# Optimization experiments

Hardware: AMD Instinct MI355X
Metric: run time of the kernel (lower is better)

## Reference

```python
import jax, jax.numpy as jnp
import numpy as np

GROUPS = 4  # init kwarg


def setup_inputs() -> dict:
    key = jax.random.key(0)
    k1, k2, k3, k4 = jax.random.split(key, 4)
    B, S, D, H = 4, 4096, 256, 10
    # 0.02 scale on weights keeps unscaled QK^T logits in a sane range
    # (original torch code uses raw randn weights and applies NO 1/sqrt(d)
    # scaling inside group_attention, which saturates softmax).
    return {
        "x": jax.random.normal(k1, (B, S, D), dtype=jnp.float32),
        "Wq": jax.random.normal(k2, (H, D, D), dtype=jnp.float32) * 0.02,
        "Wk": jax.random.normal(k3, (H, D, D), dtype=jnp.float32) * 0.02,
        "Wo": jax.random.normal(k4, (D, H * D), dtype=jnp.float32) * 0.02,
    }


def reference(x, Wq, Wk, Wo):
    # x: [B,S,D]; Wq/Wk: [H,D,D]; Wo: [D, H*D] (nn.Linear weight layout)
    H, D, _ = Wq.shape
    B, S, _ = x.shape
    G = GROUPS
    C = S // G  # chunk length

    Q = jnp.einsum('bsd,hde->hbse', x, Wq)  # [H,B,S,D]
    K = jnp.einsum('bsd,hde->hbse', x, Wk)
    # Faithful to source bug: V is projected with wk weights -> V == K

    Qg = Q.reshape(H, B, G, C, D)
    KVg = jnp.roll(K.reshape(H, B, G, C, D), shift=-1, axis=2)  # chunk i attends chunk (i+1)%G

    # NOTE: original applies NO scaling to logits (scale arg unused)
    S_ = jnp.einsum('hbgqd,hbgkd->hbgqk', Qg, KVg)   # [H,B,G,C,C]
    P = jax.nn.softmax(S_, axis=-1)
    O = jnp.einsum('hbgqk,hbgkd->hbgqd', P, KVg)     # [H,B,G,C,D]

    # concat heads on feature dim: [B,S,H*D]
    out = O.reshape(H, B, S, D).transpose(1, 2, 0, 3).reshape(B, S, H * D)
    return jnp.einsum('bsk,dk->bsd', out, Wo)  # final Linear (no bias)
```

## Files before the change

### kernel.cpp

```cpp
#include <hip/hip_runtime.h>

typedef float f32x4 __attribute__((ext_vector_type(4)));
typedef float f32x16 __attribute__((ext_vector_type(16)));
typedef short s16x8 __attribute__((ext_vector_type(8)));
typedef unsigned int u32;

#define BSZ 4
#define SEQ 4096
#define DIM 256
#define NH 10
#define NG 4
#define CHK 1024
#define BS_TOT 16384
#define HD 2560
#define LOG2E 1.44269504f

__device__ __forceinline__ unsigned short f2bf(float f) {
    unsigned int u = __builtin_bit_cast(unsigned int, f);
    u = (u + 0x7fffu + ((u >> 16) & 1u)) >> 16;
    return (unsigned short)u;
}

__device__ __forceinline__ void gload_lds16(const unsigned short* g, unsigned short* l) {
    __builtin_amdgcn_global_load_lds((const __attribute__((address_space(1))) u32*)g,
                                     (__attribute__((address_space(3))) u32*)l, 16, 0, 0);
}

__device__ __forceinline__ u32 cvtpk_bf16(float lo, float hi) {
    u32 r;
    asm("v_cvt_pk_bf16_f32 %0, %1, %2" : "=v"(r) : "v"(lo), "v"(hi));
    return r;
}


__global__ __launch_bounds__(256) void cast_f32_bf16(const float* __restrict__ s,
                                                     unsigned short* __restrict__ d, int n) {
    long i = 4L * (blockIdx.x * 256 + threadIdx.x);
    if (i < n) {
        float4 v = *(const float4*)(s + i);
        ushort4 o;
        o.x = f2bf(v.x); o.y = f2bf(v.y); o.z = f2bf(v.z); o.w = f2bf(v.w);
        *(ushort4*)(d + i) = o;
    }
}

__global__ __launch_bounds__(256) void transpose_cast_w(const float* __restrict__ Wq,
                                                        const float* __restrict__ Wk,
                                                        unsigned short* __restrict__ wqt,
                                                        unsigned short* __restrict__ wkt) {
    const float* W = (blockIdx.z & 1) ? Wk : Wq;
    unsigned short* Wt = (blockIdx.z & 1) ? wkt : wqt;
    int h = blockIdx.z >> 1;
    __shared__ float tile[32][33];
    int d0 = blockIdx.x * 32, e0 = blockIdx.y * 32;
    int tx = threadIdx.x & 31, ty = threadIdx.x >> 5;
    const float* Wh = W + (long)h * 65536;
    unsigned short* Wth = Wt + (long)h * 65536;
#pragma unroll
    for (int r = ty; r < 32; r += 8) tile[r][tx] = Wh[(long)(d0 + r) * 256 + e0 + tx];
    __syncthreads();
#pragma unroll
    for (int r = ty; r < 32; r += 8) Wth[(long)(e0 + r) * 256 + d0 + tx] = f2bf(tile[tx][r]);
}


__device__ __forceinline__ void gemm_body(const unsigned short* __restrict__ A, long lda,
                                          const unsigned short* __restrict__ Bt, long ldb,
                                          unsigned short* Cb, float* Cf, long ldc,
                                          int K, bool accum, long mbase,
                                          unsigned short* KTo, float cscale) {
    __shared__ unsigned short As[64 * 40];
    __shared__ unsigned short Bs[256 * 40];
    const int t = threadIdx.x;
    const int w = t >> 6, l = t & 63, lr = l & 15, lg = l >> 4;

    f32x4 acc[16];
#pragma unroll
    for (int i = 0; i < 16; i++) acc[i] = (f32x4){0.f, 0.f, 0.f, 0.f};

    const int ar = t >> 2, akc = (t & 3) * 8;

    for (int k0 = 0; k0 < K; k0 += 32) {
        *(s16x8*)(&As[ar * 40 + akc]) = *(const s16x8*)(A + (mbase + ar) * lda + k0 + akc);
#pragma unroll
        for (int s = 0; s < 4; s++) {
            int n = s * 64 + (t >> 2);
            *(s16x8*)(&Bs[n * 40 + akc]) = *(const s16x8*)(Bt + (long)n * ldb + k0 + akc);
        }
        __syncthreads();
        s16x8 af = *(const s16x8*)(&As[(w * 16 + lr) * 40 + lg * 8]);
        __builtin_amdgcn_s_setprio(1);
#pragma unroll
        for (int nt = 0; nt < 16; nt++) {
            s16x8 bf = *(const s16x8*)(&Bs[(nt * 16 + lr) * 40 + lg * 8]);
            acc[nt] = __builtin_amdgcn_mfma_f32_16x16x32_bf16(af, bf, acc[nt], 0, 0, 0);
        }
        __builtin_amdgcn_s_setprio(0);
        __syncthreads();
    }
    long m0 = mbase + w * 16 + lg * 4;
#pragma unroll
    for (int nt = 0; nt < 16; nt++) {
        int col = nt * 16 + lr;
#pragma unroll
        for (int r = 0; r < 4; r++) {
            long idx = (m0 + r) * ldc + col;
            if (Cb) {
                Cb[idx] = f2bf(acc[nt][r] * cscale);
            } else {
                float v = acc[nt][r];
                if (accum) v += Cf[idx];
                Cf[idx] = v;
            }
        }
    }
    if (KTo) {
        int bg = (int)(m0 >> 10);
        int key0 = (int)(m0 & 1023);
        unsigned short* base = KTo + (long)bg * (256 * 1024)
                             + (long)(key0 >> 5) * (256 * 32) + (key0 & 31);
#pragma unroll
        for (int nt = 0; nt < 16; nt++) {
            int col = nt * 16 + lr;
            ushort4 v;
            v.x = f2bf(acc[nt][0]); v.y = f2bf(acc[nt][1]);
            v.z = f2bf(acc[nt][2]); v.w = f2bf(acc[nt][3]);
            *(ushort4*)(base + (long)col * 32) = v;
        }
    }
}

__global__ __launch_bounds__(256) void proj_kernel(const unsigned short* __restrict__ xb,
                                                   const unsigned short* __restrict__ wqt,
                                                   const unsigned short* __restrict__ wkt,
                                                   unsigned short* Qb, unsigned short* Kb,
                                                   unsigned short* KTb,
                                                   int h0, long headStrideOut, long headStrideKT) {
    int h = h0 + blockIdx.y;
    bool isK = (blockIdx.z != 0);
    const unsigned short* Bt = (isK ? wkt : wqt) + (long)h * 65536;
    unsigned short* C = (isK ? Kb : Qb) + (long)blockIdx.y * headStrideOut;
    unsigned short* KTo = isK ? (KTb + (long)blockIdx.y * headStrideKT) : nullptr;
    gemm_body(xb, 256, Bt, 256, C, nullptr, 256, 256, false, (long)blockIdx.x * 64, KTo,
              isK ? 1.0f : LOG2E);
}

__global__ __launch_bounds__(256) void final_kernel(const unsigned short* __restrict__ Ob, long lda,
                                                    const unsigned short* __restrict__ wob, long ldb,
                                                    float* out, int K, int accum) {
    gemm_body(Ob, lda, wob, ldb, nullptr, out, 256, K, accum != 0, (long)blockIdx.x * 64,
              nullptr, 1.0f);
}


__global__ __launch_bounds__(256, 3) void proj128(const unsigned short* __restrict__ xb,
                                                  const unsigned short* __restrict__ wqt,
                                                  const unsigned short* __restrict__ wkt,
                                                  unsigned short* __restrict__ Qb,
                                                  unsigned short* __restrict__ Kb,
                                                  unsigned short* __restrict__ KTb,
                                                  long headStrideOut, long headStrideKT) {
    __shared__ unsigned short As[2][128 * 32];
    __shared__ unsigned short Bs[2][128 * 32];

    const int lb = blockIdx.x;
    const int logical = (lb & 7) * 640 + (lb >> 3);
    const int x = logical / 40;
    const int u = logical - x * 40;
    const int mat = u >> 1, ntile = u & 1;
    const int h = mat >> 1;
    const bool isK = (mat & 1) != 0;
    const float cs = isK ? 1.0f : LOG2E;

    const unsigned short* A = xb;
    const unsigned short* Bt = (isK ? wkt : wqt) + (long)h * 65536 + (long)ntile * 128 * 256;
    unsigned short* C = (isK ? Kb : Qb) + (long)h * headStrideOut;
    unsigned short* KTo = isK ? (KTb + (long)h * headStrideKT) : nullptr;
    const long mbase = (long)x * 128;
    const int ncol0 = ntile * 128;

    const int t = threadIdx.x, w = t >> 6, l = t & 63, lr = l & 15, lg = l >> 4;
    const int wm = w >> 1, wn = w & 1;

    int sOff[2];
#pragma unroll
    for (int i = 0; i < 2; i++) {
        int row = w * 32 + i * 16 + (l >> 2);
        int cs2 = (l & 3) ^ (row & 3);
        sOff[i] = row * 256 + cs2 * 8;
    }

    f32x4 acc[4][4];
#pragma unroll
    for (int i = 0; i < 4; i++)
#pragma unroll
        for (int j = 0; j < 4; j++) acc[i][j] = (f32x4){0.f, 0.f, 0.f, 0.f};

#define PSTAGE(buf, k0) do {                                                     \
        _Pragma("unroll")                                                        \
        for (int i = 0; i < 2; i++)                                              \
            gload_lds16(A + mbase * 256 + (k0) + sOff[i],                        \
                        &As[buf][(w * 32 + i * 16) * 32]);                       \
        _Pragma("unroll")                                                        \
        for (int i = 0; i < 2; i++)                                              \
            gload_lds16(Bt + (k0) + sOff[i],                                     \
                        &Bs[buf][(w * 32 + i * 16) * 32]);                       \
    } while (0)

    PSTAGE(0, 0);
    __syncthreads();
    int cur = 0;
    for (int ks = 0; ks < 8; ++ks) {
        if (ks < 7) PSTAGE(cur ^ 1, (ks + 1) * 32);
        s16x8 a[4], b[4];
#pragma unroll
        for (int mf = 0; mf < 4; mf++) {
            int row = wm * 64 + mf * 16 + lr;
            a[mf] = *(const s16x8*)(&As[cur][row * 32 + (lg ^ (row & 3)) * 8]);
        }
#pragma unroll
        for (int nf = 0; nf < 4; nf++) {
            int row = wn * 64 + nf * 16 + lr;
            b[nf] = *(const s16x8*)(&Bs[cur][row * 32 + (lg ^ (row & 3)) * 8]);
        }
        __builtin_amdgcn_s_setprio(1);
#pragma unroll
        for (int mf = 0; mf < 4; mf++)
#pragma unroll
            for (int nf = 0; nf < 4; nf++)
                acc[mf][nf] = __builtin_amdgcn_mfma_f32_16x16x32_bf16(a[mf], b[nf], acc[mf][nf], 0, 0, 0);
        __builtin_amdgcn_s_setprio(0);
        __syncthreads();
        cur ^= 1;
    }
#undef PSTAGE

    long m0 = mbase + wm * 64 + lg * 4;
#pragma unroll
    for (int mf = 0; mf < 4; mf++) {
        long mrow = m0 + mf * 16;
#pragma unroll
        for (int nf = 0; nf < 4; nf++) {
            int col = ncol0 + wn * 64 + nf * 16 + lr;
#pragma unroll
            for (int r = 0; r < 4; r++) C[(mrow + r) * 256 + col] = f2bf(acc[mf][nf][r] * cs);
        }
    }
    if (KTo) {
#pragma unroll
        for (int mf = 0; mf < 4; mf++) {
            long key = m0 + mf * 16;
            int bg = (int)(key >> 10), k0i = (int)(key & 1023);
            unsigned short* base = KTo + (long)bg * (256 * 1024)
                                 + (long)(k0i >> 5) * (256 * 32) + (k0i & 31);
#pragma unroll
            for (int nf = 0; nf < 4; nf++) {
                int col = ncol0 + wn * 64 + nf * 16 + lr;
                ushort4 v;
                v.x = f2bf(acc[mf][nf][0]); v.y = f2bf(acc[mf][nf][1]);
                v.z = f2bf(acc[mf][nf][2]); v.w = f2bf(acc[mf][nf][3]);
                *(ushort4*)(base + (long)col * 32) = v;
            }
        }
    }
}


__global__ __launch_bounds__(256, 3) void final128(const unsigned short* __restrict__ Ob,
                                                   long headStride,
                                                   const unsigned short* __restrict__ wob,
                                                   float* __restrict__ out) {
    __shared__ unsigned short As[2][128 * 32];
    __shared__ unsigned short Bs[2][128 * 32];

    const int lb = blockIdx.x;
    const int logical = (lb & 7) * 32 + (lb >> 3);
    const int x = logical >> 1, ntile = logical & 1;
    const long mbase = (long)x * 128;
    const int ncol0 = ntile * 128;
    const unsigned short* Bt = wob + (long)ncol0 * HD;

    const int t = threadIdx.x, w = t >> 6, l = t & 63, lr = l & 15, lg = l >> 4;
    const int wm = w >> 1, wn = w & 1;

    int sOffA[2], sOffB[2];
#pragma unroll
    for (int i = 0; i < 2; i++) {
        int row = w * 32 + i * 16 + (l >> 2);
        int cs2 = (l & 3) ^ (row & 3);
        sOffA[i] = row * 256 + cs2 * 8;
        sOffB[i] = row * HD + cs2 * 8;
    }

    f32x4 acc[4][4];
#pragma unroll
    for (int i = 0; i < 4; i++)
#pragma unroll
        for (int j = 0; j < 4; j++) acc[i][j] = (f32x4){0.f, 0.f, 0.f, 0.f};

#define FSTAGE(buf, k0) do {                                                     \
        const unsigned short* Asrc = Ob + (long)((k0) >> 8) * headStride         \
                                   + mbase * 256 + ((k0) & 255);                 \
        _Pragma("unroll")                                                        \
        for (int i = 0; i < 2; i++)                                              \
            gload_lds16(Asrc + sOffA[i], &As[buf][(w * 32 + i * 16) * 32]);      \
        _Pragma("unroll")                                                        \
        for (int i = 0; i < 2; i++)                                              \
            gload_lds16(Bt + (k0) + sOffB[i], &Bs[buf][(w * 32 + i * 16) * 32]); \
    } while (0)

    FSTAGE(0, 0);
    __syncthreads();
    int cur = 0;
    for (int ks = 0; ks < 80; ++ks) {
        if (ks < 79) FSTAGE(cur ^ 1, (ks + 1) * 32);
        s16x8 a[4], b[4];
#pragma unroll
        for (int mf = 0; mf < 4; mf++) {
            int row = wm * 64 + mf * 16 + lr;
            a[mf] = *(const s16x8*)(&As[cur][row * 32 + (lg ^ (row & 3)) * 8]);
        }
#pragma unroll
        for (int nf = 0; nf < 4; nf++) {
            int row = wn * 64 + nf * 16 + lr;
            b[nf] = *(const s16x8*)(&Bs[cur][row * 32 + (lg ^ (row & 3)) * 8]);
        }
        __builtin_amdgcn_s_setprio(1);
#pragma unroll
        for (int mf = 0; mf < 4; mf++)
#pragma unroll
            for (int nf = 0; nf < 4; nf++)
                acc[mf][nf] = __builtin_amdgcn_mfma_f32_16x16x32_bf16(a[mf], b[nf], acc[mf][nf], 0, 0, 0);
        __builtin_amdgcn_s_setprio(0);
        __syncthreads();
        cur ^= 1;
    }
#undef FSTAGE

    long m0 = mbase + wm * 64 + lg * 4;
#pragma unroll
    for (int mf = 0; mf < 4; mf++) {
        long mrow = m0 + mf * 16;
#pragma unroll
        for (int nf = 0; nf < 4; nf++) {
            int col = ncol0 + wn * 64 + nf * 16 + lr;
#pragma unroll
            for (int r = 0; r < 4; r++) out[(mrow + r) * 256 + col] = acc[mf][nf][r];
        }
    }
}


__global__ __launch_bounds__(256, 2) void attn_kernel(const unsigned short* __restrict__ Qb,
                                                      const unsigned short* __restrict__ Kb,
                                                      long headStrideQK,
                                                      const unsigned short* __restrict__ KTg,
                                                      long headStrideKT,
                                                      unsigned short* __restrict__ Ob,
                                                      long ldo, long colStride,
                                                      int chunkPerXcd) {
    const int lb = blockIdx.x;
    const int logical = (lb & 7) * chunkPerXcd + (lb >> 3);
    const int bx = logical & 7;
    const int by = (logical >> 3) & 15;
    const int h = logical >> 7;

    const unsigned short* Q = Qb + (long)h * headStrideQK;
    const unsigned short* Kp = Kb + (long)h * headStrideQK;
    const unsigned short* KT = KTg + (long)h * headStrideKT;
    unsigned short* O = Ob + (long)h * colStride;
    const int b = by >> 2, g = by & 3;
    const long qrow0 = (long)b * SEQ + (long)g * CHK + (long)bx * 128;
    const long krow0 = (long)b * SEQ + (long)((g + 1) & 3) * CHK;
    const unsigned short* KTc = KT + (long)(b * NG + ((g + 1) & 3)) * (256 * 1024);

    __shared__ unsigned short Krm[2][32 * 256];
    __shared__ unsigned short KTt[2][256 * 32];

    const int t = threadIdx.x;
    const int w = t >> 6, l = t & 63, l31 = l & 31, hi = l >> 5;

    s16x8 qf[16];
    {
        const unsigned short* qp = Q + (qrow0 + w * 32 + l31) * 256 + hi * 8;
#pragma unroll
        for (int s = 0; s < 16; s++) qf[s] = *(const s16x8*)(qp + s * 16);
    }

    f32x16 o[8];
#pragma unroll
    for (int i = 0; i < 8; i++)
#pragma unroll
        for (int j = 0; j < 16; j++) o[i][j] = 0.f;
    float l_part = 0.f;

    int kOff[4], tOff[4];
#pragma unroll
    for (int i = 0; i < 4; i++) {
        int rowK = w * 8 + i * 2 + (l >> 5);
        kOff[i] = rowK * 256 + (((l & 31) ^ (rowK & 7)) * 8);
        int rowT = w * 64 + i * 16 + (l >> 2);
        tOff[i] = rowT * 32 + (((l & 3) ^ ((rowT >> 1) & 3)) * 8);
    }

#define STAGE(buf, kt_) do {                                                    \
        const unsigned short* Ksrc = Kp + (krow0 + (long)(kt_) * 32) * 256;     \
        const unsigned short* Tsrc = KTc + (long)(kt_) * (32 * 256);            \
        _Pragma("unroll")                                                       \
        for (int i = 0; i < 4; i++)                                             \
            gload_lds16(Ksrc + kOff[i], &Krm[buf][(w * 8 + i * 2) * 256]);      \
        _Pragma("unroll")                                                       \
        for (int i = 0; i < 4; i++)                                             \
            gload_lds16(Tsrc + tOff[i], &KTt[buf][(w * 64 + i * 16) * 32]);     \
    } while (0)

    STAGE(0, 0);
    __syncthreads();
    int cur = 0;

    for (int kt = 0; kt < 32; ++kt) {
        if (kt < 31) STAGE(cur ^ 1, kt + 1);

        f32x16 st;
#pragma unroll
        for (int j = 0; j < 16; j++) st[j] = 0.f;
        __builtin_amdgcn_s_setprio(1);
#pragma unroll
        for (int ks = 0; ks < 16; ks++) {
            int col = ((2 * ks + hi) ^ (l31 & 7)) * 8;
            s16x8 kf = *(const s16x8*)(&Krm[cur][l31 * 256 + col]);
            st = __builtin_amdgcn_mfma_f32_32x32x16_bf16(kf, qf[ks], st, 0, 0, 0);
        }
        __builtin_amdgcn_s_setprio(0);

        u32 c0, c1, c2, c3, c4, c5, c6, c7;
        {
            float pa0 = __builtin_amdgcn_exp2f(st[0]),  pa1 = __builtin_amdgcn_exp2f(st[1]);
            float pa2 = __builtin_amdgcn_exp2f(st[2]),  pa3 = __builtin_amdgcn_exp2f(st[3]);
            float pa4 = __builtin_amdgcn_exp2f(st[4]),  pa5 = __builtin_amdgcn_exp2f(st[5]);
            float pa6 = __builtin_amdgcn_exp2f(st[6]),  pa7 = __builtin_amdgcn_exp2f(st[7]);
            float pa8 = __builtin_amdgcn_exp2f(st[8]),  pa9 = __builtin_amdgcn_exp2f(st[9]);
            float paA = __builtin_amdgcn_exp2f(st[10]), paB = __builtin_amdgcn_exp2f(st[11]);
            float paC = __builtin_amdgcn_exp2f(st[12]), paD = __builtin_amdgcn_exp2f(st[13]);
            float paE = __builtin_amdgcn_exp2f(st[14]), paF = __builtin_amdgcn_exp2f(st[15]);
            l_part += (((pa0 + pa1) + (pa2 + pa3)) + ((pa4 + pa5) + (pa6 + pa7)))
                    + (((pa8 + pa9) + (paA + paB)) + ((paC + paD) + (paE + paF)));
            c0 = cvtpk_bf16(pa0, pa1); c1 = cvtpk_bf16(pa2, pa3);
            c2 = cvtpk_bf16(pa4, pa5); c3 = cvtpk_bf16(pa6, pa7);
            c4 = cvtpk_bf16(pa8, pa9); c5 = cvtpk_bf16(paA, paB);
            c6 = cvtpk_bf16(paC, paD); c7 = cvtpk_bf16(paE, paF);
        }
        asm("v_permlane32_swap_b32 %0, %1" : "+v"(c0), "+v"(c2));
        asm("v_permlane32_swap_b32 %0, %1" : "+v"(c1), "+v"(c3));
        asm("v_permlane32_swap_b32 %0, %1" : "+v"(c4), "+v"(c6));
        asm("v_permlane32_swap_b32 %0, %1" : "+v"(c5), "+v"(c7));
        struct { u32 a, b, c, d; } x0 = {c0, c1, c2, c3};
        struct { u32 a, b, c, d; } x1 = {c4, c5, c6, c7};
        s16x8 pa0f = __builtin_bit_cast(s16x8, x0);
        s16x8 pa1f = __builtin_bit_cast(s16x8, x1);

        __builtin_amdgcn_s_setprio(1);
#pragma unroll
        for (int ks = 0; ks < 2; ks++) {
            s16x8 paf = ks ? pa1f : pa0f;
#pragma unroll
            for (int nt = 0; nt < 8; nt++) {
                int d = nt * 32 + l31;
                int col = ((2 * ks + hi) ^ ((d >> 1) & 3)) * 8;
                s16x8 bv = *(const s16x8*)(&KTt[cur][d * 32 + col]);
                o[nt] = __builtin_amdgcn_mfma_f32_32x32x16_bf16(paf, bv, o[nt], 0, 0, 0);
            }
        }
        __builtin_amdgcn_s_setprio(0);

        __syncthreads();
        cur ^= 1;
    }
#undef STAGE

    float lt = l_part + __shfl_xor(l_part, 32);
    float rinv = 1.0f / lt;
    float ri[16];
#pragma unroll
    for (int reg = 0; reg < 16; reg++) {
        int qr = (reg & 3) + 8 * (reg >> 2) + 4 * hi;
        ri[reg] = __shfl(rinv, qr);
    }
#pragma unroll
    for (int nt = 0; nt < 8; nt++) {
#pragma unroll
        for (int reg = 0; reg < 16; reg++) {
            int qr = (reg & 3) + 8 * (reg >> 2) + 4 * hi;
            O[(qrow0 + w * 32 + qr) * ldo + nt * 32 + l31] = f2bf(o[nt][reg] * ri[reg]);
        }
    }
}


extern "C" void kernel_launch(void* const* d_in, const int* in_sizes, int n_in,
                              void* d_out, int out_size, void* d_ws, size_t ws_size,
                              hipStream_t stream) {
    const float* x  = (const float*)d_in[0];
    const float* Wq = (const float*)d_in[1];
    const float* Wk = (const float*)d_in[2];
    const float* Wo = (const float*)d_in[3];
    float* out = (float*)d_out;
    char* ws = (char*)d_ws;

    unsigned short* xb  = (unsigned short*)(ws);
    unsigned short* wqt = (unsigned short*)(ws + 8388608);
    unsigned short* wkt = (unsigned short*)(ws + 9699328);
    unsigned short* wob = (unsigned short*)(ws + 11010048);
    char* dyn = ws + 12320768;

    cast_f32_bf16<<<4096, 256, 0, stream>>>(x, xb, BS_TOT * DIM);
    cast_f32_bf16<<<640, 256, 0, stream>>>(Wo, wob, DIM * HD);
    transpose_cast_w<<<dim3(8, 8, 2 * NH), 256, 0, stream>>>(Wq, Wk, wqt, wkt);

    const long perHeadElems = (long)BS_TOT * DIM;
    const size_t FULL_NEED = 12320768ULL + 3ULL * 83886080ULL;

    if (ws_size >= FULL_NEED) {
        unsigned short* Qb  = (unsigned short*)dyn;
        unsigned short* Kb  = Qb + (long)NH * perHeadElems;
        unsigned short* KTb = Kb + (long)NH * perHeadElems;
        proj128<<<5120, 256, 0, stream>>>(xb, wqt, wkt, Qb, Kb, KTb,
                                          perHeadElems, perHeadElems);
        attn_kernel<<<1280, 256, 0, stream>>>(Qb, Kb, perHeadElems, KTb, perHeadElems,
                                              Qb, 256, perHeadElems, 160);
        final128<<<256, 256, 0, stream>>>(Qb, perHeadElems, wob, out);
    } else {
        unsigned short* Qh  = (unsigned short*)dyn;
        unsigned short* Kh  = Qh + perHeadElems;
        unsigned short* KTh = Kh + perHeadElems;
        hipMemsetAsync(d_out, 0, (size_t)out_size * 4, stream);
        for (int h = 0; h < NH; ++h) {
            proj_kernel<<<dim3(256, 1, 2), 256, 0, stream>>>(xb, wqt, wkt, Qh, Kh, KTh, h, 0, 0);
            attn_kernel<<<128, 256, 0, stream>>>(Qh, Kh, 0, KTh, 0, Qh, 256, 0, 16);
            final_kernel<<<256, 256, 0, stream>>>(Qh, 256, wob + h * 256, HD, out, 256, 1);
        }
    }
}
```

Measured before the change: 347.1 us.

## Load V operand fragments directly from global in MFMA-ready layout, drop LDS staging

The projection kernels now write the transposed K (used as V) in a fragment-major layout, so each lane's 16-byte MFMA B-operand is contiguous. The attention kernel then loads the V fragments straight from global into registers instead of staging them through LDS, which halves LDS usage and removes the LDS reads for the PV matmul. The QK^T chain is also split into two independent accumulators to break the MFMA dependency chain. Occupancy hint is lowered to 1 block per CU to make room for 16 extra register vectors, at the cost of latency hiding, and the global loads are issued each iteration without prefetch.

```diff
diff --git a/kernel.cpp b/kernel.cpp
--- a/kernel.cpp
+++ b/kernel.cpp
@@ -31,6 +31,7 @@
     asm("v_cvt_pk_bf16_f32 %0, %1, %2" : "=v"(r) : "v"(lo), "v"(hi));
     return r;
 }
+
 
 
 __global__ __launch_bounds__(256) void cast_f32_bf16(const float* __restrict__ s,
@@ -117,15 +118,16 @@
     if (KTo) {
         int bg = (int)(m0 >> 10);
         int key0 = (int)(m0 & 1023);
-        unsigned short* base = KTo + (long)bg * (256 * 1024)
-                             + (long)(key0 >> 5) * (256 * 32) + (key0 & 31);
+        int kt = key0 >> 5, kw = key0 & 31;
+        unsigned short* base = KTo + (long)bg * (256 * 1024) + (long)kt * 8192
+                             + (kw >> 4) * 512 + ((kw >> 3) & 1) * 256 + (kw & 7);
 #pragma unroll
         for (int nt = 0; nt < 16; nt++) {
             int col = nt * 16 + lr;
             ushort4 v;
             v.x = f2bf(acc[nt][0]); v.y = f2bf(acc[nt][1]);
             v.z = f2bf(acc[nt][2]); v.w = f2bf(acc[nt][3]);
-            *(ushort4*)(base + (long)col * 32) = v;
+            *(ushort4*)(base + (col >> 5) * 1024 + (col & 31) * 8) = v;
         }
     }
 }
@@ -250,16 +252,17 @@
 #pragma unroll
         for (int mf = 0; mf < 4; mf++) {
             long key = m0 + mf * 16;
-            int bg = (int)(key >> 10), k0i = (int)(key & 1023);
-            unsigned short* base = KTo + (long)bg * (256 * 1024)
-                                 + (long)(k0i >> 5) * (256 * 32) + (k0i & 31);
+            int bg = (int)(key >> 10), k1 = (int)(key & 1023);
+            int kt = k1 >> 5, kw = k1 & 31;
+            unsigned short* base = KTo + (long)bg * (256 * 1024) + (long)kt * 8192
+                                 + (kw >> 4) * 512 + ((kw >> 3) & 1) * 256 + (kw & 7);
 #pragma unroll
             for (int nf = 0; nf < 4; nf++) {
                 int col = ncol0 + wn * 64 + nf * 16 + lr;
                 ushort4 v;
                 v.x = f2bf(acc[mf][nf][0]); v.y = f2bf(acc[mf][nf][1]);
                 v.z = f2bf(acc[mf][nf][2]); v.w = f2bf(acc[mf][nf][3]);
-                *(ushort4*)(base + (long)col * 32) = v;
+                *(ushort4*)(base + (col >> 5) * 1024 + (col & 31) * 8) = v;
             }
         }
     }
@@ -351,7 +354,7 @@
 }
 
 
-__global__ __launch_bounds__(256, 2) void attn_kernel(const unsigned short* __restrict__ Qb,
+__global__ __launch_bounds__(256, 1) void attn_kernel(const unsigned short* __restrict__ Qb,
                                                       const unsigned short* __restrict__ Kb,
                                                       long headStrideQK,
                                                       const unsigned short* __restrict__ KTg,
@@ -375,7 +378,6 @@
     const unsigned short* KTc = KT + (long)(b * NG + ((g + 1) & 3)) * (256 * 1024);
 
     __shared__ unsigned short Krm[2][32 * 256];
-    __shared__ unsigned short KTt[2][256 * 32];
 
     const int t = threadIdx.x;
     const int w = t >> 6, l = t & 63, l31 = l & 31, hi = l >> 5;
@@ -394,24 +396,18 @@
         for (int j = 0; j < 16; j++) o[i][j] = 0.f;
     float l_part = 0.f;
 
-    int kOff[4], tOff[4];
+    int kOff[4];
 #pragma unroll
     for (int i = 0; i < 4; i++) {
         int rowK = w * 8 + i * 2 + (l >> 5);
         kOff[i] = rowK * 256 + (((l & 31) ^ (rowK & 7)) * 8);
-        int rowT = w * 64 + i * 16 + (l >> 2);
-        tOff[i] = rowT * 32 + (((l & 3) ^ ((rowT >> 1) & 3)) * 8);
     }
 
 #define STAGE(buf, kt_) do {                                                    \
         const unsigned short* Ksrc = Kp + (krow0 + (long)(kt_) * 32) * 256;     \
-        const unsigned short* Tsrc = KTc + (long)(kt_) * (32 * 256);            \
         _Pragma("unroll")                                                       \
         for (int i = 0; i < 4; i++)                                             \
             gload_lds16(Ksrc + kOff[i], &Krm[buf][(w * 8 + i * 2) * 256]);      \
-        _Pragma("unroll")                                                       \
-        for (int i = 0; i < 4; i++)                                             \
-            gload_lds16(Tsrc + tOff[i], &KTt[buf][(w * 64 + i * 16) * 32]);     \
     } while (0)
 
     STAGE(0, 0);
@@ -421,28 +417,47 @@
     for (int kt = 0; kt < 32; ++kt) {
         if (kt < 31) STAGE(cur ^ 1, kt + 1);
 
-        f32x16 st;
-#pragma unroll
-        for (int j = 0; j < 16; j++) st[j] = 0.f;
+        const unsigned short* Tsrc = KTc + (long)kt * 8192 + l * 8;
+        s16x8 vv[16];
+#pragma unroll
+        for (int ks = 0; ks < 2; ks++)
+#pragma unroll
+            for (int nt = 0; nt < 8; nt++)
+                vv[ks * 8 + nt] = *(const s16x8*)(Tsrc + (nt * 2 + ks) * 512);
+
+        f32x16 stA, stB;
+#pragma unroll
+        for (int j = 0; j < 16; j++) { stA[j] = 0.f; stB[j] = 0.f; }
         __builtin_amdgcn_s_setprio(1);
 #pragma unroll
-        for (int ks = 0; ks < 16; ks++) {
-            int col = ((2 * ks + hi) ^ (l31 & 7)) * 8;
-            s16x8 kf = *(const s16x8*)(&Krm[cur][l31 * 256 + col]);
-            st = __builtin_amdgcn_mfma_f32_32x32x16_bf16(kf, qf[ks], st, 0, 0, 0);
+        for (int s = 0; s < 8; s++) {
+            int cA = ((2 * s + hi) ^ (l31 & 7)) * 8;
+            int cB = ((2 * (s + 8) + hi) ^ (l31 & 7)) * 8;
+            s16x8 kfA = *(const s16x8*)(&Krm[cur][l31 * 256 + cA]);
+            s16x8 kfB = *(const s16x8*)(&Krm[cur][l31 * 256 + cB]);
+            stA = __builtin_amdgcn_mfma_f32_32x32x16_bf16(kfA, qf[s], stA, 0, 0, 0);
+            stB = __builtin_amdgcn_mfma_f32_32x32x16_bf16(kfB, qf[s + 8], stB, 0, 0, 0);
         }
         __builtin_amdgcn_s_setprio(0);
 
         u32 c0, c1, c2, c3, c4, c5, c6, c7;
         {
-            float pa0 = __builtin_amdgcn_exp2f(st[0]),  pa1 = __builtin_amdgcn_exp2f(st[1]);
-            float pa2 = __builtin_amdgcn_exp2f(st[2]),  pa3 = __builtin_amdgcn_exp2f(st[3]);
-            float pa4 = __builtin_amdgcn_exp2f(st[4]),  pa5 = __builtin_amdgcn_exp2f(st[5]);
-            float pa6 = __builtin_amdgcn_exp2f(st[6]),  pa7 = __builtin_amdgcn_exp2f(st[7]);
-            float pa8 = __builtin_amdgcn_exp2f(st[8]),  pa9 = __builtin_amdgcn_exp2f(st[9]);
-            float paA = __builtin_amdgcn_exp2f(st[10]), paB = __builtin_amdgcn_exp2f(st[11]);
-            float paC = __builtin_amdgcn_exp2f(st[12]), paD = __builtin_amdgcn_exp2f(st[13]);
-            float paE = __builtin_amdgcn_exp2f(st[14]), paF = __builtin_amdgcn_exp2f(st[15]);
+            float pa0 = __builtin_amdgcn_exp2f(stA[0] + stB[0]);
+            float pa1 = __builtin_amdgcn_exp2f(stA[1] + stB[1]);
+            float pa2 = __builtin_amdgcn_exp2f(stA[2] + stB[2]);
+            float pa3 = __builtin_amdgcn_exp2f(stA[3] + stB[3]);
+            float pa4 = __builtin_amdgcn_exp2f(stA[4] + stB[4]);
+            float pa5 = __builtin_amdgcn_exp2f(stA[5] + stB[5]);
+            float pa6 = __builtin_amdgcn_exp2f(stA[6] + stB[6]);
+            float pa7 = __builtin_amdgcn_exp2f(stA[7] + stB[7]);
+            float pa8 = __builtin_amdgcn_exp2f(stA[8] + stB[8]);
+            float pa9 = __builtin_amdgcn_exp2f(stA[9] + stB[9]);
+            float paA = __builtin_amdgcn_exp2f(stA[10] + stB[10]);
+            float paB = __builtin_amdgcn_exp2f(stA[11] + stB[11]);
+            float paC = __builtin_amdgcn_exp2f(stA[12] + stB[12]);
+            float paD = __builtin_amdgcn_exp2f(stA[13] + stB[13]);
+            float paE = __builtin_amdgcn_exp2f(stA[14] + stB[14]);
+            float paF = __builtin_amdgcn_exp2f(stA[15] + stB[15]);
             l_part += (((pa0 + pa1) + (pa2 + pa3)) + ((pa4 + pa5) + (pa6 + pa7)))
                     + (((pa8 + pa9) + (paA + paB)) + ((paC + paD) + (paE + paF)));
             c0 = cvtpk_bf16(pa0, pa1); c1 = cvtpk_bf16(pa2, pa3);
@@ -461,16 +476,11 @@
 
         __builtin_amdgcn_s_setprio(1);
 #pragma unroll
-        for (int ks = 0; ks < 2; ks++) {
-            s16x8 paf = ks ? pa1f : pa0f;
-#pragma unroll
-            for (int nt = 0; nt < 8; nt++) {
-                int d = nt * 32 + l31;
-                int col = ((2 * ks + hi) ^ ((d >> 1) & 3)) * 8;
-                s16x8 bv = *(const s16x8*)(&KTt[cur][d * 32 + col]);
-                o[nt] = __builtin_amdgcn_mfma_f32_32x32x16_bf16(paf, bv, o[nt], 0, 0, 0);
-            }
-        }
+        for (int nt = 0; nt < 8; nt++)
+            o[nt] = __builtin_amdgcn_mfma_f32_32x32x16_bf16(pa0f, vv[nt], o[nt], 0, 0, 0);
+#pragma unroll
+        for (int nt = 0; nt < 8; nt++)
+            o[nt] = __builtin_amdgcn_mfma_f32_32x32x16_bf16(pa1f, vv[8 + nt], o[nt], 0, 0, 0);
         __builtin_amdgcn_s_setprio(0);
 
         __syncthreads();
```

Result: slower. 428.0 us (+23.3%).

## Pre-tile K and V in MFMA fragment order so attention loads are contiguous

Applied to the files above, without the earlier changes.

The projection kernels now write K in two fragment-ordered tiled layouts: one matching the QK^T MFMA operand, one matching the PV operand. Each lane can then read its 16-byte fragment at a linear offset. The attention kernel stages each 32-key tile with contiguous global_load_lds copies and reads LDS with simple lane-linear addressing, dropping the XOR-swizzle address math and the row-major K buffer. The cost is scattered 2-byte stores in the projection epilogue for the K-operand layout, plus changed Q head striding that relies on colStride equalling the old head stride.

```diff
diff --git a/kernel.cpp b/kernel.cpp
--- a/kernel.cpp
+++ b/kernel.cpp
@@ -31,6 +31,7 @@
     asm("v_cvt_pk_bf16_f32 %0, %1, %2" : "=v"(r) : "v"(lo), "v"(hi));
     return r;
 }
+
 
 
 __global__ __launch_bounds__(256) void cast_f32_bf16(const float* __restrict__ s,
@@ -68,7 +69,8 @@
                                           const unsigned short* __restrict__ Bt, long ldb,
                                           unsigned short* Cb, float* Cf, long ldc,
                                           int K, bool accum, long mbase,
-                                          unsigned short* KTo, float cscale) {
+                                          unsigned short* KQo, unsigned short* KTo,
+                                          float cscale) {
     __shared__ unsigned short As[64 * 40];
     __shared__ unsigned short Bs[256 * 40];
     const int t = threadIdx.x;
@@ -99,33 +101,49 @@
         __syncthreads();
     }
     long m0 = mbase + w * 16 + lg * 4;
-#pragma unroll
-    for (int nt = 0; nt < 16; nt++) {
-        int col = nt * 16 + lr;
-#pragma unroll
-        for (int r = 0; r < 4; r++) {
-            long idx = (m0 + r) * ldc + col;
-            if (Cb) {
-                Cb[idx] = f2bf(acc[nt][r] * cscale);
-            } else {
-                float v = acc[nt][r];
-                if (accum) v += Cf[idx];
-                Cf[idx] = v;
+    if (Cb || Cf) {
+#pragma unroll
+        for (int nt = 0; nt < 16; nt++) {
+            int col = nt * 16 + lr;
+#pragma unroll
+            for (int r = 0; r < 4; r++) {
+                long idx = (m0 + r) * ldc + col;
+                if (Cb) {
+                    Cb[idx] = f2bf(acc[nt][r] * cscale);
+                } else {
+                    float v = acc[nt][r];
+                    if (accum) v += Cf[idx];
+                    Cf[idx] = v;
+                }
             }
+        }
+    }
+    if (KQo) {
+        int bg = (int)(m0 >> 10);
+        int kin = (int)(m0 & 1023);
+        int kt = kin >> 5, kw = kin & 31;
+        unsigned short* tb = KQo + (long)bg * (256 * 1024) + (long)kt * 8192;
+#pragma unroll
+        for (int nt = 0; nt < 16; nt++) {
+            int d = nt * 16 + lr;
+            unsigned short* p = tb + (d >> 4) * 512 + ((d >> 3) & 1) * 256 + (d & 7);
+#pragma unroll
+            for (int r = 0; r < 4; r++) p[(kw + r) * 8] = f2bf(acc[nt][r]);
         }
     }
     if (KTo) {
         int bg = (int)(m0 >> 10);
         int key0 = (int)(m0 & 1023);
-        unsigned short* base = KTo + (long)bg * (256 * 1024)
-                             + (long)(key0 >> 5) * (256 * 32) + (key0 & 31);
+        int kt = key0 >> 5, kw = key0 & 31;
+        unsigned short* base = KTo + (long)bg * (256 * 1024) + (long)kt * 8192
+                             + (kw >> 4) * 512 + ((kw >> 3) & 1) * 256 + (kw & 7);
 #pragma unroll
         for (int nt = 0; nt < 16; nt++) {
             int col = nt * 16 + lr;
             ushort4 v;
             v.x = f2bf(acc[nt][0]); v.y = f2bf(acc[nt][1]);
             v.z = f2bf(acc[nt][2]); v.w = f2bf(acc[nt][3]);
-            *(ushort4*)(base + (long)col * 32) = v;
+            *(ushort4*)(base + (col >> 5) * 1024 + (col & 31) * 8) = v;
         }
     }
 }
@@ -133,23 +151,24 @@
 __global__ __launch_bounds__(256) void proj_kernel(const unsigned short* __restrict__ xb,
                                                    const unsigned short* __restrict__ wqt,
                                                    const unsigned short* __restrict__ wkt,
-                                                   unsigned short* Qb, unsigned short* Kb,
+                                                   unsigned short* Qb, unsigned short* KQb,
                                                    unsigned short* KTb,
                                                    int h0, long headStrideOut, long headStrideKT) {
     int h = h0 + blockIdx.y;
     bool isK = (blockIdx.z != 0);
     const unsigned short* Bt = (isK ? wkt : wqt) + (long)h * 65536;
-    unsigned short* C = (isK ? Kb : Qb) + (long)blockIdx.y * headStrideOut;
+    unsigned short* C = isK ? nullptr : (Qb + (long)blockIdx.y * headStrideOut);
+    unsigned short* KQo = isK ? (KQb + (long)blockIdx.y * headStrideKT) : nullptr;
     unsigned short* KTo = isK ? (KTb + (long)blockIdx.y * headStrideKT) : nullptr;
-    gemm_body(xb, 256, Bt, 256, C, nullptr, 256, 256, false, (long)blockIdx.x * 64, KTo,
-              isK ? 1.0f : LOG2E);
+    gemm_body(xb, 256, Bt, 256, C, nullptr, 256, 256, false, (long)blockIdx.x * 64,
+              KQo, KTo, isK ? 1.0f : LOG2E);
 }
 
 __global__ __launch_bounds__(256) void final_kernel(const unsigned short* __restrict__ Ob, long lda,
                                                     const unsigned short* __restrict__ wob, long ldb,
                                                     float* out, int K, int accum) {
     gemm_body(Ob, lda, wob, ldb, nullptr, out, 256, K, accum != 0, (long)blockIdx.x * 64,
-              nullptr, 1.0f);
+              nullptr, nullptr, 1.0f);
 }
 
 
@@ -157,7 +176,7 @@
                                                   const unsigned short* __restrict__ wqt,
                                                   const unsigned short* __restrict__ wkt,
                                                   unsigned short* __restrict__ Qb,
-                                                  unsigned short* __restrict__ Kb,
+                                                  unsigned short* __restrict__ KQb,
                                                   unsigned short* __restrict__ KTb,
                                                   long headStrideOut, long headStrideKT) {
     __shared__ unsigned short As[2][128 * 32];
@@ -170,12 +189,9 @@
     const int mat = u >> 1, ntile = u & 1;
     const int h = mat >> 1;
     const bool isK = (mat & 1) != 0;
-    const float cs = isK ? 1.0f : LOG2E;
 
     const unsigned short* A = xb;
     const unsigned short* Bt = (isK ? wkt : wqt) + (long)h * 65536 + (long)ntile * 128 * 256;
-    unsigned short* C = (isK ? Kb : Qb) + (long)h * headStrideOut;
-    unsigned short* KTo = isK ? (KTb + (long)h * headStrideKT) : nullptr;
     const long mbase = (long)x * 128;
     const int ncol0 = ntile * 128;
 
@@ -236,30 +252,40 @@
 #undef PSTAGE
 
     long m0 = mbase + wm * 64 + lg * 4;
-#pragma unroll
-    for (int mf = 0; mf < 4; mf++) {
-        long mrow = m0 + mf * 16;
-#pragma unroll
-        for (int nf = 0; nf < 4; nf++) {
-            int col = ncol0 + wn * 64 + nf * 16 + lr;
-#pragma unroll
-            for (int r = 0; r < 4; r++) C[(mrow + r) * 256 + col] = f2bf(acc[mf][nf][r] * cs);
-        }
-    }
-    if (KTo) {
+    if (!isK) {
+        unsigned short* C = Qb + (long)h * headStrideOut;
+#pragma unroll
+        for (int mf = 0; mf < 4; mf++) {
+            long mrow = m0 + mf * 16;
+#pragma unroll
+            for (int nf = 0; nf < 4; nf++) {
+                int col = ncol0 + wn * 64 + nf * 16 + lr;
+#pragma unroll
+                for (int r = 0; r < 4; r++)
+                    C[(mrow + r) * 256 + col] = f2bf(acc[mf][nf][r] * LOG2E);
+            }
+        }
+    } else {
+        unsigned short* KQo = KQb + (long)h * headStrideKT;
+        unsigned short* KTo = KTb + (long)h * headStrideKT;
 #pragma unroll
         for (int mf = 0; mf < 4; mf++) {
             long key = m0 + mf * 16;
-            int bg = (int)(key >> 10), k0i = (int)(key & 1023);
-            unsigned short* base = KTo + (long)bg * (256 * 1024)
-                                 + (long)(k0i >> 5) * (256 * 32) + (k0i & 31);
+            int bg = (int)(key >> 10), kin = (int)(key & 1023);
+            int kt = kin >> 5, kw = kin & 31;
+            unsigned short* qtb = KQo + (long)bg * (256 * 1024) + (long)kt * 8192;
+            unsigned short* vtb = KTo + (long)bg * (256 * 1024) + (long)kt * 8192
+                                + (kw >> 4) * 512 + ((kw >> 3) & 1) * 256 + (kw & 7);
 #pragma unroll
             for (int nf = 0; nf < 4; nf++) {
-                int col = ncol0 + wn * 64 + nf * 16 + lr;
+                int d = ncol0 + wn * 64 + nf * 16 + lr;
+                unsigned short* p = qtb + (d >> 4) * 512 + ((d >> 3) & 1) * 256 + (d & 7);
+#pragma unroll
+                for (int r = 0; r < 4; r++) p[(kw + r) * 8] = f2bf(acc[mf][nf][r]);
                 ushort4 v;
                 v.x = f2bf(acc[mf][nf][0]); v.y = f2bf(acc[mf][nf][1]);
                 v.z = f2bf(acc[mf][nf][2]); v.w = f2bf(acc[mf][nf][3]);
-                *(ushort4*)(base + (long)col * 32) = v;
+                *(ushort4*)(vtb + (d >> 5) * 1024 + (d & 31) * 8) = v;
             }
         }
     }
@@ -352,7 +378,7 @@
 
 
 __global__ __launch_bounds__(256, 2) void attn_kernel(const unsigned short* __restrict__ Qb,
-                                                      const unsigned short* __restrict__ Kb,
+                                                      const unsigned short* __restrict__ KQg,
                                                       long headStrideQK,
                                                       const unsigned short* __restrict__ KTg,
                                                       long headStrideKT,
@@ -365,17 +391,18 @@
     const int by = (logical >> 3) & 15;
     const int h = logical >> 7;
 
-    const unsigned short* Q = Qb + (long)h * headStrideQK;
-    const unsigned short* Kp = Kb + (long)h * headStrideQK;
+    const unsigned short* Q = Qb + (long)h * colStride;
+    const unsigned short* KQ = KQg + (long)h * headStrideQK;
     const unsigned short* KT = KTg + (long)h * headStrideKT;
     unsigned short* O = Ob + (long)h * colStride;
     const int b = by >> 2, g = by & 3;
     const long qrow0 = (long)b * SEQ + (long)g * CHK + (long)bx * 128;
-    const long krow0 = (long)b * SEQ + (long)((g + 1) & 3) * CHK;
-    const unsigned short* KTc = KT + (long)(b * NG + ((g + 1) & 3)) * (256 * 1024);
-
-    __shared__ unsigned short Krm[2][32 * 256];
-    __shared__ unsigned short KTt[2][256 * 32];
+    const int bgk = b * NG + ((g + 1) & 3);
+    const unsigned short* KQc = KQ + (long)bgk * (256 * 1024);
+    const unsigned short* KTc = KT + (long)bgk * (256 * 1024);
+
+    __shared__ unsigned short Klds[2][8192];
+    __shared__ unsigned short Vlds[2][8192];
 
     const int t = threadIdx.x;
     const int w = t >> 6, l = t & 63, l31 = l & 31, hi = l >> 5;
@@ -394,24 +421,15 @@
         for (int j = 0; j < 16; j++) o[i][j] = 0.f;
     float l_part = 0.f;
 
-    int kOff[4], tOff[4];
-#pragma unroll
-    for (int i = 0; i < 4; i++) {
-        int rowK = w * 8 + i * 2 + (l >> 5);
-        kOff[i] = rowK * 256 + (((l & 31) ^ (rowK & 7)) * 8);
-        int rowT = w * 64 + i * 16 + (l >> 2);
-        tOff[i] = rowT * 32 + (((l & 3) ^ ((rowT >> 1) & 3)) * 8);
-    }
-
 #define STAGE(buf, kt_) do {                                                    \
-        const unsigned short* Ksrc = Kp + (krow0 + (long)(kt_) * 32) * 256;     \
-        const unsigned short* Tsrc = KTc + (long)(kt_) * (32 * 256);            \
+        const unsigned short* Ks = KQc + (long)(kt_) * 8192 + l * 8;            \
+        const unsigned short* Vs = KTc + (long)(kt_) * 8192 + l * 8;            \
         _Pragma("unroll")                                                       \
-        for (int i = 0; i < 4; i++)                                             \
-            gload_lds16(Ksrc + kOff[i], &Krm[buf][(w * 8 + i * 2) * 256]);      \
-        _Pragma("unroll")                                                       \
-        for (int i = 0; i < 4; i++)                                             \
-            gload_lds16(Tsrc + tOff[i], &KTt[buf][(w * 64 + i * 16) * 32]);     \
+        for (int i = 0; i < 4; i++) {                                           \
+            int c = w * 4 + i;                                                  \
+            gload_lds16(Ks + c * 512, &Klds[buf][c * 512]);                     \
+            gload_lds16(Vs + c * 512, &Vlds[buf][c * 512]);                     \
+        }                                                                       \
     } while (0)
 
     STAGE(0, 0);
@@ -427,8 +445,7 @@
         __builtin_amdgcn_s_setprio(1);
 #pragma unroll
         for (int ks = 0; ks < 16; ks++) {
-            int col = ((2 * ks + hi) ^ (l31 & 7)) * 8;
-            s16x8 kf = *(const s16x8*)(&Krm[cur][l31 * 256 + col]);
+            s16x8 kf = *(const s16x8*)(&Klds[cur][ks * 512 + l * 8]);
             st = __builtin_amdgcn_mfma_f32_32x32x16_bf16(kf, qf[ks], st, 0, 0, 0);
         }
         __builtin_amdgcn_s_setprio(0);
@@ -465,9 +482,7 @@
             s16x8 paf = ks ? pa1f : pa0f;
 #pragma unroll
             for (int nt = 0; nt < 8; nt++) {
-                int d = nt * 32 + l31;
-                int col = ((2 * ks + hi) ^ ((d >> 1) & 3)) * 8;
-                s16x8 bv = *(const s16x8*)(&KTt[cur][d * 32 + col]);
+                s16x8 bv = *(const s16x8*)(&Vlds[cur][(nt * 2 + ks) * 512 + l * 8]);
                 o[nt] = __builtin_amdgcn_mfma_f32_32x32x16_bf16(paf, bv, o[nt], 0, 0, 0);
             }
         }
@@ -522,21 +537,21 @@
 
     if (ws_size >= FULL_NEED) {
         unsigned short* Qb  = (unsigned short*)dyn;
-        unsigned short* Kb  = Qb + (long)NH * perHeadElems;
-        unsigned short* KTb = Kb + (long)NH * perHeadElems;
-        proj128<<<5120, 256, 0, stream>>>(xb, wqt, wkt, Qb, Kb, KTb,
+        unsigned short* KQb = Qb + (long)NH * perHeadElems;
+        unsigned short* KTb = KQb + (long)NH * perHeadElems;
+        proj128<<<5120, 256, 0, stream>>>(xb, wqt, wkt, Qb, KQb, KTb,
                                           perHeadElems, perHeadElems);
-        attn_kernel<<<1280, 256, 0, stream>>>(Qb, Kb, perHeadElems, KTb, perHeadElems,
+        attn_kernel<<<1280, 256, 0, stream>>>(Qb, KQb, perHeadElems, KTb, perHeadElems,
                                               Qb, 256, perHeadElems, 160);
         final128<<<256, 256, 0, stream>>>(Qb, perHeadElems, wob, out);
     } else {
         unsigned short* Qh  = (unsigned short*)dyn;
-        unsigned short* Kh  = Qh + perHeadElems;
-        unsigned short* KTh = Kh + perHeadElems;
+        unsigned short* KQh = Qh + perHeadElems;
+        unsigned short* KTh = KQh + perHeadElems;
         hipMemsetAsync(d_out, 0, (size_t)out_size * 4, stream);
         for (int h = 0; h < NH; ++h) {
-            proj_kernel<<<dim3(256, 1, 2), 256, 0, stream>>>(xb, wqt, wkt, Qh, Kh, KTh, h, 0, 0);
-            attn_kernel<<<128, 256, 0, stream>>>(Qh, Kh, 0, KTh, 0, Qh, 256, 0, 16);
+            proj_kernel<<<dim3(256, 1, 2), 256, 0, stream>>>(xb, wqt, wkt, Qh, KQh, KTh, h, 0, 0);
+            attn_kernel<<<128, 256, 0, stream>>>(Qh, KQh, 0, KTh, 0, Qh, 256, 0, 16);
             final_kernel<<<256, 256, 0, stream>>>(Qh, 256, wob + h * 256, HD, out, 256, 1);
         }
     }
```

Measured after the change: 344.0 us. Within noise of the previous version (-0.9%).
